# Kernel optimization log

Hardware: AMD Instinct MI355X
Metric: run time of the kernel (lower is better)

## Reference

```python
import jax, jax.numpy as jnp
import numpy as np

TARGET_RADIUS = 0.99
EPS = 1e-8


def _spectral_norm_wh(W_h):
    # 3-step power iteration (detached, as in torch no_grad), then scale W_h
    # so its spectral radius is ~TARGET_RADIUS. sigma keeps grad through W_h.
    D = W_h.shape[0]
    u = jax.random.normal(jax.random.key(42), (D,), dtype=W_h.dtype)
    u = u / jnp.linalg.norm(u)
    Wd = jax.lax.stop_gradient(W_h)
    v = u
    for _ in range(3):
        v = Wd.T @ u
        v = v / (jnp.linalg.norm(v) + EPS)
        u = Wd @ v
        u = u / (jnp.linalg.norm(u) + EPS)
    sigma = jnp.abs(u @ W_h @ v)
    return W_h * (TARGET_RADIUS / (sigma + EPS))


def setup_inputs() -> dict:
    key = jax.random.key(0)
    T, B, D = 256, 64, 2048
    ks = jax.random.split(key, 5)
    std = 0.02  # ~xavier scale for D=2048 is sqrt(2/(2D))~0.022
    return {
        "x": jax.random.normal(ks[0], (T, B, D), dtype=jnp.float32),
        "z": jax.random.normal(ks[1], (T, B, D), dtype=jnp.float32),
        "h0": jnp.zeros((B, D), dtype=jnp.float32),
        "W_x": jax.random.normal(ks[2], (D, D), dtype=jnp.float32) * std,
        "W_h": jax.random.normal(ks[3], (D, D), dtype=jnp.float32) * std,
        "W_gate": jax.random.normal(ks[4], (D, D), dtype=jnp.float32) * std,
        "b": jnp.zeros((D,), dtype=jnp.float32),
    }


def reference(x, z, h0, W_x, W_h, W_gate, b):
    # h_t = tanh(W_x@x_t + (W_h@h_{t-1}) * sigmoid(W_gate@x_t) + b)
    # out_t = h_t * silu(z_t)
    W_h_eff = _spectral_norm_wh(W_h)
    # Precompute input projections as one big GEMM over T*B (same math).
    xWx = jnp.einsum("tbd,ed->tbe", x, W_x) + b          # [T,B,D]
    gate = jax.nn.sigmoid(jnp.einsum("tbd,ed->tbe", x, W_gate))  # [T,B,D]
    silu_z = jax.nn.silu(z)                               # [T,B,D]

    def step(h_prev, inp):
        xw_t, g_t, sz_t = inp
        Rh = h_prev @ W_h_eff.T                           # [B,D]
        h_new = jnp.tanh(xw_t + Rh * g_t)
        out_t = h_new * sz_t
        return h_new, (h_new, out_t)

    _, (hs, output) = jax.lax.scan(step, h0, (xWx, gate, silu_z))
    h = jnp.concatenate([h0[None], hs], axis=0)           # [T+1,B,D]
    return output, h
```

## Files before the change

### kernel.cpp

```cpp
#include <hip/hip_runtime.h>
#include <cstdint>
#include <cmath>


#define THREEFRY_PARTITIONABLE 1

static constexpr int Tt = 256;
static constexpr int Bb = 64;
static constexpr int Dk = 2048;
static constexpr int Mrows = Tt * Bb;
static constexpr float EPSF = 1e-8f;
static constexpr float TARGET_RADIUS = 0.99f;

__device__ __forceinline__ void tf_round(uint32_t& x0, uint32_t& x1, int r) {
    x0 += x1;
    x1 = (x1 << r) | (x1 >> (32 - r));
    x1 ^= x0;
}

__device__ __forceinline__ uint2 threefry2x32(uint32_t ks0, uint32_t ks1,
                                              uint32_t x0, uint32_t x1) {
    uint32_t ks2 = ks0 ^ ks1 ^ 0x1BD11BDAu;
    x0 += ks0; x1 += ks1;
    tf_round(x0,x1,13); tf_round(x0,x1,15); tf_round(x0,x1,26); tf_round(x0,x1,6);
    x0 += ks1; x1 += ks2 + 1u;
    tf_round(x0,x1,17); tf_round(x0,x1,29); tf_round(x0,x1,16); tf_round(x0,x1,24);
    x0 += ks2; x1 += ks0 + 2u;
    tf_round(x0,x1,13); tf_round(x0,x1,15); tf_round(x0,x1,26); tf_round(x0,x1,6);
    x0 += ks0; x1 += ks1 + 3u;
    tf_round(x0,x1,17); tf_round(x0,x1,29); tf_round(x0,x1,16); tf_round(x0,x1,24);
    x0 += ks1; x1 += ks2 + 4u;
    tf_round(x0,x1,13); tf_round(x0,x1,15); tf_round(x0,x1,26); tf_round(x0,x1,6);
    x0 += ks2; x1 += ks0 + 5u;
    return make_uint2(x0, x1);
}

__global__ __launch_bounds__(256) void k_rng(float* __restrict__ u) {
    __shared__ float red[256];
    __shared__ float s_inv;
    float local = 0.f;
    for (int i = threadIdx.x; i < Dk; i += 256) {
        uint32_t bits;
#if THREEFRY_PARTITIONABLE
        uint2 r = threefry2x32(0u, 42u, 0u, (uint32_t)i);
        bits = r.x ^ r.y;
#else
        if (i < Dk / 2) {
            uint2 r = threefry2x32(0u, 42u, (uint32_t)i, (uint32_t)(i + Dk / 2));
            bits = r.x;
        } else {
            uint2 r = threefry2x32(0u, 42u, (uint32_t)(i - Dk / 2), (uint32_t)i);
            bits = r.y;
        }
#endif
        uint32_t fb = (bits >> 9) | 0x3f800000u;
        float f01 = __uint_as_float(fb) - 1.0f;
        const float lo = -0.99999994f;
        float uu = f01 * (1.0f - lo) + lo;
        uu = fmaxf(lo, uu);
        float g = 1.41421356237f * erfinvf(uu);
        u[i] = g;
        local += g * g;
    }
    red[threadIdx.x] = local;
    __syncthreads();
    for (int s = 128; s > 0; s >>= 1) {
        if (threadIdx.x < s) red[threadIdx.x] += red[threadIdx.x + s];
        __syncthreads();
    }
    if (threadIdx.x == 0) s_inv = 1.0f / sqrtf(red[0]);
    __syncthreads();
    float inv = s_inv;
    for (int i = threadIdx.x; i < Dk; i += 256) u[i] *= inv;
}

__global__ __launch_bounds__(256) void k_matvec_T(const float* __restrict__ W,
                                                  const float* __restrict__ u,
                                                  float* __restrict__ out) {
    __shared__ float us[Dk];
    for (int i = threadIdx.x; i < Dk; i += 256) us[i] = u[i];
    __syncthreads();
    int j = blockIdx.x * 256 + threadIdx.x;
    float acc = 0.f;
    for (int i = 0; i < Dk; ++i) acc += W[(size_t)i * Dk + j] * us[i];
    out[j] = acc;
}

__global__ __launch_bounds__(256) void k_matvec_N(const float* __restrict__ W,
                                                  const float* __restrict__ v,
                                                  float* __restrict__ out) {
    __shared__ float red[256];
    const float* Wr = W + (size_t)blockIdx.x * Dk;
    float acc = 0.f;
    for (int j = threadIdx.x; j < Dk; j += 256) acc += Wr[j] * v[j];
    red[threadIdx.x] = acc;
    __syncthreads();
    for (int s = 128; s > 0; s >>= 1) {
        if (threadIdx.x < s) red[threadIdx.x] += red[threadIdx.x + s];
        __syncthreads();
    }
    if (threadIdx.x == 0) out[blockIdx.x] = red[0];
}

__global__ __launch_bounds__(256) void k_normalize(float* __restrict__ vec) {
    __shared__ float red[256];
    __shared__ float s_inv;
    float acc = 0.f;
    for (int i = threadIdx.x; i < Dk; i += 256) { float x = vec[i]; acc += x * x; }
    red[threadIdx.x] = acc;
    __syncthreads();
    for (int s = 128; s > 0; s >>= 1) {
        if (threadIdx.x < s) red[threadIdx.x] += red[threadIdx.x + s];
        __syncthreads();
    }
    if (threadIdx.x == 0) s_inv = 1.0f / (sqrtf(red[0]) + EPSF);
    __syncthreads();
    float inv = s_inv;
    for (int i = threadIdx.x; i < Dk; i += 256) vec[i] *= inv;
}

__global__ __launch_bounds__(256) void k_sigma(const float* __restrict__ uraw,
                                               float* __restrict__ scale_out) {
    __shared__ float red[256];
    float acc = 0.f;
    for (int i = threadIdx.x; i < Dk; i += 256) { float x = uraw[i]; acc += x * x; }
    red[threadIdx.x] = acc;
    __syncthreads();
    for (int s = 128; s > 0; s >>= 1) {
        if (threadIdx.x < s) red[threadIdx.x] += red[threadIdx.x + s];
        __syncthreads();
    }
    if (threadIdx.x == 0) {
        float ss = red[0];
        float n = sqrtf(ss);
        float sigma = ss / (n + EPSF);
        scale_out[0] = TARGET_RADIUS / (sigma + EPSF);
    }
}

__global__ __launch_bounds__(256) void k_dualgemm(const float* __restrict__ X,
                                                  const float* __restrict__ Wx,
                                                  const float* __restrict__ Wg,
                                                  const float* __restrict__ bias,
                                                  float* __restrict__ xw_out,
                                                  float* __restrict__ gate_out) {
    __shared__ float As[16][68];
    __shared__ float Bxs[16][68];
    __shared__ float Bgs[16][68];

    const int tid = threadIdx.x;
    const int bm = blockIdx.x;
    const int bn = blockIdx.y;
    const int tx = tid & 15;
    const int ty = tid >> 4;

    float accX[4][4] = {};
    float accG[4][4] = {};

    const int lrow = tid >> 2;
    const int lk4  = (tid & 3) * 4;
    const float* Xp  = X  + (size_t)(bm * 64 + lrow) * Dk + lk4;
    const float* Wxp = Wx + (size_t)(bn * 64 + lrow) * Dk + lk4;
    const float* Wgp = Wg + (size_t)(bn * 64 + lrow) * Dk + lk4;

    for (int k0 = 0; k0 < Dk; k0 += 16) {
        float4 xa  = *(const float4*)(Xp  + k0);
        float4 wxa = *(const float4*)(Wxp + k0);
        float4 wga = *(const float4*)(Wgp + k0);
        __syncthreads();
        As [lk4 + 0][lrow] = xa.x;  As [lk4 + 1][lrow] = xa.y;
        As [lk4 + 2][lrow] = xa.z;  As [lk4 + 3][lrow] = xa.w;
        Bxs[lk4 + 0][lrow] = wxa.x; Bxs[lk4 + 1][lrow] = wxa.y;
        Bxs[lk4 + 2][lrow] = wxa.z; Bxs[lk4 + 3][lrow] = wxa.w;
        Bgs[lk4 + 0][lrow] = wga.x; Bgs[lk4 + 1][lrow] = wga.y;
        Bgs[lk4 + 2][lrow] = wga.z; Bgs[lk4 + 3][lrow] = wga.w;
        __syncthreads();
#pragma unroll
        for (int kk = 0; kk < 16; ++kk) {
            const float4 a  = *(const float4*)&As [kk][ty * 4];
            const float4 bx = *(const float4*)&Bxs[kk][tx * 4];
            const float4 bg = *(const float4*)&Bgs[kk][tx * 4];
            float av[4]  = {a.x, a.y, a.z, a.w};
            float bxv[4] = {bx.x, bx.y, bx.z, bx.w};
            float bgv[4] = {bg.x, bg.y, bg.z, bg.w};
#pragma unroll
            for (int i = 0; i < 4; ++i)
#pragma unroll
                for (int j = 0; j < 4; ++j) {
                    accX[i][j] += av[i] * bxv[j];
                    accG[i][j] += av[i] * bgv[j];
                }
        }
    }

    const int m0 = bm * 64 + ty * 4;
    const int n0 = bn * 64 + tx * 4;
    float4 bv = *(const float4*)(bias + n0);
#pragma unroll
    for (int i = 0; i < 4; ++i) {
        float4 xo, go;
        xo.x = accX[i][0] + bv.x; xo.y = accX[i][1] + bv.y;
        xo.z = accX[i][2] + bv.z; xo.w = accX[i][3] + bv.w;
        go.x = 1.0f / (1.0f + expf(-accG[i][0]));
        go.y = 1.0f / (1.0f + expf(-accG[i][1]));
        go.z = 1.0f / (1.0f + expf(-accG[i][2]));
        go.w = 1.0f / (1.0f + expf(-accG[i][3]));
        *(float4*)(xw_out   + (size_t)(m0 + i) * Dk + n0) = xo;
        *(float4*)(gate_out + (size_t)(m0 + i) * Dk + n0) = go;
    }
}

__global__ __launch_bounds__(256) void k_step(const float* __restrict__ Wh,
                                              const float* __restrict__ scale_p,
                                              const float* __restrict__ z_t,
                                              float* __restrict__ xw_t,
                                              const float* __restrict__ h_prev,
                                              float* __restrict__ hg_t) {
    __shared__ float Hs[32][36];
    __shared__ float Ws[32][36];
    const int tid = threadIdx.x;
    const int bn = blockIdx.x;
    const int bb = blockIdx.y;
    const int tx = tid & 15;
    const int ty = tid >> 4;

    float a00 = 0.f, a01 = 0.f, a10 = 0.f, a11 = 0.f;

    const int lrow = tid >> 3;
    const int lk4  = (tid & 7) * 4;
    const float* Hp = h_prev + (size_t)(bb * 32 + lrow) * Dk + lk4;
    const float* Wp = Wh     + (size_t)(bn * 32 + lrow) * Dk + lk4;

    for (int k0 = 0; k0 < Dk; k0 += 32) {
        float4 ha = *(const float4*)(Hp + k0);
        float4 wa = *(const float4*)(Wp + k0);
        __syncthreads();
        Hs[lk4 + 0][lrow] = ha.x; Hs[lk4 + 1][lrow] = ha.y;
        Hs[lk4 + 2][lrow] = ha.z; Hs[lk4 + 3][lrow] = ha.w;
        Ws[lk4 + 0][lrow] = wa.x; Ws[lk4 + 1][lrow] = wa.y;
        Ws[lk4 + 2][lrow] = wa.z; Ws[lk4 + 3][lrow] = wa.w;
        __syncthreads();
#pragma unroll
        for (int kk = 0; kk < 32; ++kk) {
            float2 hv = *(const float2*)&Hs[kk][ty * 2];
            float2 wv = *(const float2*)&Ws[kk][tx * 2];
            a00 += hv.x * wv.x; a01 += hv.x * wv.y;
            a10 += hv.y * wv.x; a11 += hv.y * wv.y;
        }
    }

    const float sc = scale_p[0];
    const int e0 = bn * 32 + tx * 2;
    const int b0 = bb * 32 + ty * 2;
    float acc[2][2] = {{a00, a01}, {a10, a11}};
#pragma unroll
    for (int i = 0; i < 2; ++i)
#pragma unroll
        for (int j = 0; j < 2; ++j) {
            size_t idx = (size_t)(b0 + i) * Dk + (e0 + j);
            float Rh = acc[i][j] * sc;
            float g = hg_t[idx];
            float pre = xw_t[idx] + Rh * g;
            float hn = tanhf(pre);
            float zv = z_t[idx];
            float sz = zv / (1.0f + expf(-zv));
            hg_t[idx] = hn;
            xw_t[idx] = hn * sz;
        }
}

extern "C" void kernel_launch(void* const* d_in, const int* in_sizes, int n_in,
                              void* d_out, int out_size, void* d_ws, size_t ws_size,
                              hipStream_t stream) {
    const float* x    = (const float*)d_in[0];
    const float* z    = (const float*)d_in[1];
    const float* h0   = (const float*)d_in[2];
    const float* Wx   = (const float*)d_in[3];
    const float* Wh   = (const float*)d_in[4];
    const float* Wg   = (const float*)d_in[5];
    const float* bias = (const float*)d_in[6];

    float* out  = (float*)d_out;
    float* hbuf = out + (size_t)Tt * Bb * Dk;

    float* ws    = (float*)d_ws;
    float* u     = ws;
    float* v     = ws + 2048;
    float* tmp   = ws + 4096;
    float* scale = ws + 6144;

    const size_t BD = (size_t)Bb * Dk;

    hipMemcpyAsync(hbuf, h0, BD * sizeof(float), hipMemcpyDeviceToDevice, stream);

    k_rng<<<1, 256, 0, stream>>>(u);
    float* uc = u;
    float* ut = tmp;
    for (int it = 0; it < 3; ++it) {
        k_matvec_T<<<8, 256, 0, stream>>>(Wh, uc, v);
        k_normalize<<<1, 256, 0, stream>>>(v);
        k_matvec_N<<<2048, 256, 0, stream>>>(Wh, v, ut);
        if (it < 2) {
            k_normalize<<<1, 256, 0, stream>>>(ut);
            float* t2 = uc; uc = ut; ut = t2;
        }
    }
    k_sigma<<<1, 256, 0, stream>>>(ut, scale);

    dim3 gg(Mrows / 64, Dk / 64);
    k_dualgemm<<<gg, 256, 0, stream>>>(x, Wx, Wg, bias, out, hbuf + BD);

    dim3 gs(Dk / 32, Bb / 32);
    for (int t = 0; t < Tt; ++t) {
        k_step<<<gs, 256, 0, stream>>>(Wh, scale,
                                       z + (size_t)t * BD,
                                       out + (size_t)t * BD,
                                       hbuf + (size_t)t * BD,
                                       hbuf + (size_t)(t + 1) * BD);
    }
}
```

Measured before the change: 19.75 ms.

## Fuse recurrence into persistent cooperative kernel and enlarge dual-GEMM tiles

```diff
diff --git a/kernel.cpp b/kernel.cpp
--- a/kernel.cpp
+++ b/kernel.cpp
@@ -1,9 +1,10 @@
 #include <hip/hip_runtime.h>
+#include <hip/hip_cooperative_groups.h>
 #include <cstdint>
 #include <cmath>
 
-
-#define THREEFRY_PARTITIONABLE 1
+namespace cg = cooperative_groups;
+
 
 static constexpr int Tt = 256;
 static constexpr int Bb = 64;
@@ -40,19 +41,8 @@
     __shared__ float s_inv;
     float local = 0.f;
     for (int i = threadIdx.x; i < Dk; i += 256) {
-        uint32_t bits;
-#if THREEFRY_PARTITIONABLE
         uint2 r = threefry2x32(0u, 42u, 0u, (uint32_t)i);
-        bits = r.x ^ r.y;
-#else
-        if (i < Dk / 2) {
-            uint2 r = threefry2x32(0u, 42u, (uint32_t)i, (uint32_t)(i + Dk / 2));
-            bits = r.x;
-        } else {
-            uint2 r = threefry2x32(0u, 42u, (uint32_t)(i - Dk / 2), (uint32_t)i);
-            bits = r.y;
-        }
-#endif
+        uint32_t bits = r.x ^ r.y;
         uint32_t fb = (bits >> 9) | 0x3f800000u;
         float f01 = __uint_as_float(fb) - 1.0f;
         const float lo = -0.99999994f;
@@ -138,15 +128,15 @@
     }
 }
 
-__global__ __launch_bounds__(256) void k_dualgemm(const float* __restrict__ X,
-                                                  const float* __restrict__ Wx,
-                                                  const float* __restrict__ Wg,
-                                                  const float* __restrict__ bias,
-                                                  float* __restrict__ xw_out,
-                                                  float* __restrict__ gate_out) {
-    __shared__ float As[16][68];
-    __shared__ float Bxs[16][68];
-    __shared__ float Bgs[16][68];
+__global__ __launch_bounds__(256, 2) void k_dualgemm(const float* __restrict__ X,
+                                                     const float* __restrict__ Wx,
+                                                     const float* __restrict__ Wg,
+                                                     const float* __restrict__ bias,
+                                                     float* __restrict__ xw_out,
+                                                     float* __restrict__ gate_out) {
+    __shared__ float As [16][132];
+    __shared__ float Bxs[16][132];
+    __shared__ float Bgs[16][132];
 
     const int tid = threadIdx.x;
     const int bm = blockIdx.x;
@@ -154,119 +144,154 @@
     const int tx = tid & 15;
     const int ty = tid >> 4;
 
-    float accX[4][4] = {};
-    float accG[4][4] = {};
+    float accX[8][8] = {};
+    float accG[8][8] = {};
 
     const int lrow = tid >> 2;
-    const int lk4  = (tid & 3) * 4;
-    const float* Xp  = X  + (size_t)(bm * 64 + lrow) * Dk + lk4;
-    const float* Wxp = Wx + (size_t)(bn * 64 + lrow) * Dk + lk4;
-    const float* Wgp = Wg + (size_t)(bn * 64 + lrow) * Dk + lk4;
+    const int lk4  = (tid & 3) << 2;
+    const float* Xp0  = X  + (size_t)(bm * 128 + lrow) * Dk + lk4;
+    const float* Xp1  = Xp0 + (size_t)64 * Dk;
+    const float* Wxp0 = Wx + (size_t)(bn * 128 + lrow) * Dk + lk4;
+    const float* Wxp1 = Wxp0 + (size_t)64 * Dk;
+    const float* Wgp0 = Wg + (size_t)(bn * 128 + lrow) * Dk + lk4;
+    const float* Wgp1 = Wgp0 + (size_t)64 * Dk;
 
     for (int k0 = 0; k0 < Dk; k0 += 16) {
-        float4 xa  = *(const float4*)(Xp  + k0);
-        float4 wxa = *(const float4*)(Wxp + k0);
-        float4 wga = *(const float4*)(Wgp + k0);
-        __syncthreads();
-        As [lk4 + 0][lrow] = xa.x;  As [lk4 + 1][lrow] = xa.y;
-        As [lk4 + 2][lrow] = xa.z;  As [lk4 + 3][lrow] = xa.w;
-        Bxs[lk4 + 0][lrow] = wxa.x; Bxs[lk4 + 1][lrow] = wxa.y;
-        Bxs[lk4 + 2][lrow] = wxa.z; Bxs[lk4 + 3][lrow] = wxa.w;
-        Bgs[lk4 + 0][lrow] = wga.x; Bgs[lk4 + 1][lrow] = wga.y;
-        Bgs[lk4 + 2][lrow] = wga.z; Bgs[lk4 + 3][lrow] = wga.w;
+        float4 xa0 = *(const float4*)(Xp0  + k0);
+        float4 xa1 = *(const float4*)(Xp1  + k0);
+        float4 wx0 = *(const float4*)(Wxp0 + k0);
+        float4 wx1 = *(const float4*)(Wxp1 + k0);
+        float4 wg0 = *(const float4*)(Wgp0 + k0);
+        float4 wg1 = *(const float4*)(Wgp1 + k0);
+        __syncthreads();
+        As [lk4 + 0][lrow]      = xa0.x; As [lk4 + 1][lrow]      = xa0.y;
+        As [lk4 + 2][lrow]      = xa0.z; As [lk4 + 3][lrow]      = xa0.w;
+        As [lk4 + 0][lrow + 64] = xa1.x; As [lk4 + 1][lrow + 64] = xa1.y;
+        As [lk4 + 2][lrow + 64] = xa1.z; As [lk4 + 3][lrow + 64] = xa1.w;
+        Bxs[lk4 + 0][lrow]      = wx0.x; Bxs[lk4 + 1][lrow]      = wx0.y;
+        Bxs[lk4 + 2][lrow]      = wx0.z; Bxs[lk4 + 3][lrow]      = wx0.w;
+        Bxs[lk4 + 0][lrow + 64] = wx1.x; Bxs[lk4 + 1][lrow + 64] = wx1.y;
+        Bxs[lk4 + 2][lrow + 64] = wx1.z; Bxs[lk4 + 3][lrow + 64] = wx1.w;
+        Bgs[lk4 + 0][lrow]      = wg0.x; Bgs[lk4 + 1][lrow]      = wg0.y;
+        Bgs[lk4 + 2][lrow]      = wg0.z; Bgs[lk4 + 3][lrow]      = wg0.w;
+        Bgs[lk4 + 0][lrow + 64] = wg1.x; Bgs[lk4 + 1][lrow + 64] = wg1.y;
+        Bgs[lk4 + 2][lrow + 64] = wg1.z; Bgs[lk4 + 3][lrow + 64] = wg1.w;
         __syncthreads();
 #pragma unroll
         for (int kk = 0; kk < 16; ++kk) {
-            const float4 a  = *(const float4*)&As [kk][ty * 4];
-            const float4 bx = *(const float4*)&Bxs[kk][tx * 4];
-            const float4 bg = *(const float4*)&Bgs[kk][tx * 4];
-            float av[4]  = {a.x, a.y, a.z, a.w};
-            float bxv[4] = {bx.x, bx.y, bx.z, bx.w};
-            float bgv[4] = {bg.x, bg.y, bg.z, bg.w};
+            const float4 a0 = *(const float4*)&As [kk][ty * 8];
+            const float4 a1 = *(const float4*)&As [kk][ty * 8 + 4];
+            const float4 x0 = *(const float4*)&Bxs[kk][tx * 8];
+            const float4 x1 = *(const float4*)&Bxs[kk][tx * 8 + 4];
+            const float4 g0 = *(const float4*)&Bgs[kk][tx * 8];
+            const float4 g1 = *(const float4*)&Bgs[kk][tx * 8 + 4];
+            float av[8] = {a0.x, a0.y, a0.z, a0.w, a1.x, a1.y, a1.z, a1.w};
+            float xv[8] = {x0.x, x0.y, x0.z, x0.w, x1.x, x1.y, x1.z, x1.w};
+            float gv[8] = {g0.x, g0.y, g0.z, g0.w, g1.x, g1.y, g1.z, g1.w};
 #pragma unroll
-            for (int i = 0; i < 4; ++i)
+            for (int i = 0; i < 8; ++i)
 #pragma unroll
-                for (int j = 0; j < 4; ++j) {
-                    accX[i][j] += av[i] * bxv[j];
-                    accG[i][j] += av[i] * bgv[j];
+                for (int j = 0; j < 8; ++j) {
+                    accX[i][j] = fmaf(av[i], xv[j], accX[i][j]);
+                    accG[i][j] = fmaf(av[i], gv[j], accG[i][j]);
                 }
         }
     }
 
-    const int m0 = bm * 64 + ty * 4;
-    const int n0 = bn * 64 + tx * 4;
-    float4 bv = *(const float4*)(bias + n0);
+    const int m0 = bm * 128 + ty * 8;
+    const int n0 = bn * 128 + tx * 8;
+    float4 bv0 = *(const float4*)(bias + n0);
+    float4 bv1 = *(const float4*)(bias + n0 + 4);
 #pragma unroll
-    for (int i = 0; i < 4; ++i) {
-        float4 xo, go;
-        xo.x = accX[i][0] + bv.x; xo.y = accX[i][1] + bv.y;
-        xo.z = accX[i][2] + bv.z; xo.w = accX[i][3] + bv.w;
-        go.x = 1.0f / (1.0f + expf(-accG[i][0]));
-        go.y = 1.0f / (1.0f + expf(-accG[i][1]));
-        go.z = 1.0f / (1.0f + expf(-accG[i][2]));
-        go.w = 1.0f / (1.0f + expf(-accG[i][3]));
-        *(float4*)(xw_out   + (size_t)(m0 + i) * Dk + n0) = xo;
-        *(float4*)(gate_out + (size_t)(m0 + i) * Dk + n0) = go;
-    }
-}
-
-__global__ __launch_bounds__(256) void k_step(const float* __restrict__ Wh,
-                                              const float* __restrict__ scale_p,
-                                              const float* __restrict__ z_t,
-                                              float* __restrict__ xw_t,
-                                              const float* __restrict__ h_prev,
-                                              float* __restrict__ hg_t) {
-    __shared__ float Hs[32][36];
-    __shared__ float Ws[32][36];
+    for (int i = 0; i < 8; ++i) {
+        float4 xo0, xo1, go0, go1;
+        xo0.x = accX[i][0] + bv0.x; xo0.y = accX[i][1] + bv0.y;
+        xo0.z = accX[i][2] + bv0.z; xo0.w = accX[i][3] + bv0.w;
+        xo1.x = accX[i][4] + bv1.x; xo1.y = accX[i][5] + bv1.y;
+        xo1.z = accX[i][6] + bv1.z; xo1.w = accX[i][7] + bv1.w;
+        go0.x = 1.0f / (1.0f + expf(-accG[i][0]));
+        go0.y = 1.0f / (1.0f + expf(-accG[i][1]));
+        go0.z = 1.0f / (1.0f + expf(-accG[i][2]));
+        go0.w = 1.0f / (1.0f + expf(-accG[i][3]));
+        go1.x = 1.0f / (1.0f + expf(-accG[i][4]));
+        go1.y = 1.0f / (1.0f + expf(-accG[i][5]));
+        go1.z = 1.0f / (1.0f + expf(-accG[i][6]));
+        go1.w = 1.0f / (1.0f + expf(-accG[i][7]));
+        float* xrow = xw_out   + (size_t)(m0 + i) * Dk + n0;
+        float* grow = gate_out + (size_t)(m0 + i) * Dk + n0;
+        *(float4*)xrow       = xo0;
+        *(float4*)(xrow + 4) = xo1;
+        *(float4*)grow       = go0;
+        *(float4*)(grow + 4) = go1;
+    }
+}
+
+__global__ __launch_bounds__(256) void k_recur(const float* __restrict__ Wh,
+                                               const float* __restrict__ scale_p,
+                                               const float* __restrict__ z,
+                                               float* __restrict__ out,
+                                               float* __restrict__ hbuf) {
+    cg::grid_group grid = cg::this_grid();
+    __shared__ float Ws[8][2564];
+
     const int tid = threadIdx.x;
-    const int bn = blockIdx.x;
-    const int bb = blockIdx.y;
-    const int tx = tid & 15;
-    const int ty = tid >> 4;
-
-    float a00 = 0.f, a01 = 0.f, a10 = 0.f, a11 = 0.f;
-
-    const int lrow = tid >> 3;
-    const int lk4  = (tid & 7) * 4;
-    const float* Hp = h_prev + (size_t)(bb * 32 + lrow) * Dk + lk4;
-    const float* Wp = Wh     + (size_t)(bn * 32 + lrow) * Dk + lk4;
-
-    for (int k0 = 0; k0 < Dk; k0 += 32) {
-        float4 ha = *(const float4*)(Hp + k0);
-        float4 wa = *(const float4*)(Wp + k0);
-        __syncthreads();
-        Hs[lk4 + 0][lrow] = ha.x; Hs[lk4 + 1][lrow] = ha.y;
-        Hs[lk4 + 2][lrow] = ha.z; Hs[lk4 + 3][lrow] = ha.w;
-        Ws[lk4 + 0][lrow] = wa.x; Ws[lk4 + 1][lrow] = wa.y;
-        Ws[lk4 + 2][lrow] = wa.z; Ws[lk4 + 3][lrow] = wa.w;
-        __syncthreads();
-#pragma unroll
-        for (int kk = 0; kk < 32; ++kk) {
-            float2 hv = *(const float2*)&Hs[kk][ty * 2];
-            float2 wv = *(const float2*)&Ws[kk][tx * 2];
-            a00 += hv.x * wv.x; a01 += hv.x * wv.y;
-            a10 += hv.y * wv.x; a11 += hv.y * wv.y;
+    const int e0 = blockIdx.x * 8;
+    const float sc = scale_p[0];
+
+    for (int idx = tid; idx < 8 * 512; idx += 256) {
+        const int r = idx >> 9;
+        const int c = (idx & 511) << 2;
+        float4 w = *(const float4*)(Wh + (size_t)(e0 + r) * Dk + c);
+        Ws[r][c + 0] = w.x * sc; Ws[r][c + 1] = w.y * sc;
+        Ws[r][c + 2] = w.z * sc; Ws[r][c + 3] = w.w * sc;
+    }
+    __syncthreads();
+
+    const int e = tid & 7;
+    const int brow = tid >> 3;
+    const float* wr = &Ws[e][0];
+    const size_t BD = (size_t)Bb * Dk;
+    const size_t i0 = (size_t)brow * Dk + e0 + e;
+    const size_t i1 = i0 + (size_t)32 * Dk;
+
+    for (int t = 0; t < Tt; ++t) {
+        const float* hbase = hbuf + (size_t)t * BD;
+        float* hg = hbuf + (size_t)(t + 1) * BD;
+        float* xo = out  + (size_t)t * BD;
+        const float* zt = z + (size_t)t * BD;
+
+        float g0 = hg[i0], g1 = hg[i1];
+        float x0 = xo[i0], x1 = xo[i1];
+        float z0 = zt[i0], z1 = zt[i1];
+
+        const float* hp0 = hbase + (size_t)brow * Dk;
+        const float* hp1 = hp0 + (size_t)32 * Dk;
+        float s00 = 0.f, s01 = 0.f, s10 = 0.f, s11 = 0.f;
+#pragma unroll 4
+        for (int d = 0; d < Dk; d += 8) {
+            float4 w0 = *(const float4*)(wr + d);
+            float4 w1 = *(const float4*)(wr + d + 4);
+            float4 a0 = *(const float4*)(hp0 + d);
+            float4 a1 = *(const float4*)(hp0 + d + 4);
+            float4 b0 = *(const float4*)(hp1 + d);
+            float4 b1 = *(const float4*)(hp1 + d + 4);
+            s00 = fmaf(a0.w, w0.w, fmaf(a0.z, w0.z, fmaf(a0.y, w0.y, fmaf(a0.x, w0.x, s00))));
+            s01 = fmaf(a1.w, w1.w, fmaf(a1.z, w1.z, fmaf(a1.y, w1.y, fmaf(a1.x, w1.x, s01))));
+            s10 = fmaf(b0.w, w0.w, fmaf(b0.z, w0.z, fmaf(b0.y, w0.y, fmaf(b0.x, w0.x, s10))));
+            s11 = fmaf(b1.w, w1.w, fmaf(b1.z, w1.z, fmaf(b1.y, w1.y, fmaf(b1.x, w1.x, s11))));
         }
-    }
-
-    const float sc = scale_p[0];
-    const int e0 = bn * 32 + tx * 2;
-    const int b0 = bb * 32 + ty * 2;
-    float acc[2][2] = {{a00, a01}, {a10, a11}};
-#pragma unroll
-    for (int i = 0; i < 2; ++i)
-#pragma unroll
-        for (int j = 0; j < 2; ++j) {
-            size_t idx = (size_t)(b0 + i) * Dk + (e0 + j);
-            float Rh = acc[i][j] * sc;
-            float g = hg_t[idx];
-            float pre = xw_t[idx] + Rh * g;
-            float hn = tanhf(pre);
-            float zv = z_t[idx];
-            float sz = zv / (1.0f + expf(-zv));
-            hg_t[idx] = hn;
-            xw_t[idx] = hn * sz;
-        }
+        float r0 = s00 + s01;
+        float r1 = s10 + s11;
+
+        float hn0 = tanhf(x0 + r0 * g0);
+        float hn1 = tanhf(x1 + r1 * g1);
+        float sz0 = z0 / (1.0f + expf(-z0));
+        float sz1 = z1 / (1.0f + expf(-z1));
+        hg[i0] = hn0; xo[i0] = hn0 * sz0;
+        hg[i1] = hn1; xo[i1] = hn1 * sz1;
+
+        if (t + 1 < Tt) grid.sync();
+    }
 }
 
 extern "C" void kernel_launch(void* const* d_in, const int* in_sizes, int n_in,
@@ -307,15 +332,17 @@
     }
     k_sigma<<<1, 256, 0, stream>>>(ut, scale);
 
-    dim3 gg(Mrows / 64, Dk / 64);
+    dim3 gg(Mrows / 128, Dk / 128);
     k_dualgemm<<<gg, 256, 0, stream>>>(x, Wx, Wg, bias, out, hbuf + BD);
 
-    dim3 gs(Dk / 32, Bb / 32);
-    for (int t = 0; t < Tt; ++t) {
-        k_step<<<gs, 256, 0, stream>>>(Wh, scale,
-                                       z + (size_t)t * BD,
-                                       out + (size_t)t * BD,
-                                       hbuf + (size_t)t * BD,
-                                       hbuf + (size_t)(t + 1) * BD);
-    }
-}
+    {
+        const float* aWh = Wh;
+        const float* aSc = scale;
+        const float* aZ  = z;
+        float* aOut = out;
+        float* aH   = hbuf;
+        void* kargs[] = {(void*)&aWh, (void*)&aSc, (void*)&aZ,
+                         (void*)&aOut, (void*)&aH};
+        hipLaunchCooperativeKernel(k_recur, dim3(256), dim3(256), kargs, 0, stream);
+    }
+}
```

Measured after the change: 20.04 ms. No clear change (+1.5%).
